# Performance work log

Measured on AMD Instinct MI355X. Metric: run time of the kernel, lower is better.

## Reference

```python
import jax, jax.numpy as jnp
import numpy as np

EPS = 1e-10      # normalizer eps from the torch module
IN_EPS = 1e-5    # torch InstanceNorm2d default eps
STRIDE = 2
PAD = 1


def _dw_conv_transpose(x, W):
    """Depthwise ConvTranspose2d applied for every output channel at once.

    x: [B, Cin, H, W]
    W: [Cin, Cout, kh, kw]  (W[:, i] is sub_convs[i].weight of shape [Cin, 1, kh, kw])
    returns: [B, Cin, Cout, H', W'] where channel (c, i) = convT of x[:, c] with W[c, i].
    """
    Cin, Cout, kh, kw = W.shape
    # Transposed conv == dilated conv with spatially flipped kernel,
    # lhs_dilation = stride, padding = k - 1 - pad (output_padding = 0).
    rhs = jnp.flip(W, axis=(-2, -1)).reshape(Cin * Cout, 1, kh, kw)
    pad_h = (kh - 1 - PAD, kh - 1 - PAD)
    pad_w = (kw - 1 - PAD, kw - 1 - PAD)
    out = jax.lax.conv_general_dilated(
        x, rhs,
        window_strides=(1, 1),
        padding=(pad_h, pad_w),
        lhs_dilation=(STRIDE, STRIDE),
        dimension_numbers=('NCHW', 'OIHW', 'NCHW'),
        feature_group_count=Cin,
    )  # [B, Cin*Cout, H', W'], group-major: group c -> channels c*Cout:(c+1)*Cout
    B = x.shape[0]
    return out.reshape(B, Cin, Cout, out.shape[2], out.shape[3])


def setup_inputs() -> dict:
    key = jax.random.key(0)
    k1, k2, k3 = jax.random.split(key, 3)
    B, Cin, Cout, H, Wd, K = 2, 64, 64, 48, 48, 4
    x = jax.random.normal(k1, (B, Cin, H, Wd), dtype=jnp.float32)
    # Positive-leaning weights keep the normalizer (convT of ones) away from zero.
    W = 0.05 + 0.1 * jax.random.uniform(k2, (Cin, Cout, K, K), dtype=jnp.float32)
    bias = 0.02 * jax.random.normal(k3, (Cout,), dtype=jnp.float32)
    return {"x": x, "W": W, "bias": bias}


def reference(x, W, bias):
    # numerator: depthwise convT of the input for every (in_ch, out_ch) pair
    num = _dw_conv_transpose(x, W)                       # [B, Cin, Cout, H', W']
    # normalizer: same convT applied to ones (batch-independent -> batch of 1)
    den = _dw_conv_transpose(jnp.ones_like(x[:1]), W) + EPS  # [1, Cin, Cout, H', W']
    out = jnp.sum(num / den, axis=1) + bias[None, :, None, None]  # [B, Cout, H', W']
    # InstanceNorm2d (no affine, biased variance) over spatial dims per (b, c)
    mean = jnp.mean(out, axis=(2, 3), keepdims=True)
    var = jnp.var(out, axis=(2, 3), keepdims=True)
    return (out - mean) / jnp.sqrt(var + IN_EPS)
```

## Files before the change

### kernel.cpp

```cpp
#include <hip/hip_runtime.h>

#define BB    2
#define CIN   64
#define NI    64
#define HIN   48
#define WIN   48
#define HO    96
#define WO    96
#define EPSN  1e-10f
#define IN_EPS 1e-5f
#define IMG   (HO*WO)
#define NIMG  (BB*NI)

#define TW    52
#define TROWS 50
#define TILE  (TROWS*TW)

__device__ float g_F[NI * CIN * 16];
__device__ float g_R[NI * CIN * 16];

__global__ __launch_bounds__(256) void prep_kernel(const float* __restrict__ Wt) {
    const int e = blockIdx.x * 256 + threadIdx.x;
    const int i = e >> 6, c = e & 63;
    float w[16];
    const float* wp = Wt + ((size_t)c * NI + i) * 16;
#pragma unroll
    for (int j = 0; j < 16; ++j) w[j] = wp[j];
    float* F = g_F + (size_t)e * 16;
    float* R = g_R + (size_t)e * 16;
#pragma unroll
    for (int j = 0; j < 16; ++j) {
        const int py = (j >> 3) & 1, px = (j >> 2) & 1, a = (j >> 1) & 1, bb = j & 1;
        const int kh = py ? (a ? 2 : 0) : (a ? 3 : 1);
        const int kw = px ? (bb ? 2 : 0) : (bb ? 3 : 1);
        const int r0 = py ? 0 : 1, r1 = py ? 2 : 3;
        const int q0 = px ? 0 : 1, q1 = px ? 2 : 3;
        const float den = w[r0 * 4 + q0] + w[r0 * 4 + q1]
                        + w[r1 * 4 + q0] + w[r1 * 4 + q1];
        F[j] = w[kh * 4 + kw] / (den + EPSN);
        const int cy = j >> 2, cx = j & 3;
        const int THn[4] = {1, 2, 2, 1};
        const int THv[4][2] = {{1, 1}, {0, 2}, {1, 3}, {2, 2}};
        float den2 = 0.f;
        for (int aa = 0; aa < THn[cy]; ++aa)
            for (int bb2 = 0; bb2 < THn[cx]; ++bb2)
                den2 += w[THv[cy][aa] * 4 + THv[cx][bb2]];
        R[j] = 1.f / (den2 + EPSN);
    }
}

template <int CS>
__global__ __launch_bounds__(192, 2) void conv_kernel(
        const float* __restrict__ x, const float* __restrict__ Wt,
        const float* __restrict__ bias, float* __restrict__ part) {
    constexpr int NC = CIN / CS;
    const int bi = blockIdx.x, s = blockIdx.y;
    const int b = bi >> 6, i = bi & 63, c0 = s * NC;
    const int tid = threadIdx.x;
    const int ty = tid / 12, tx = tid - 12 * ty;

    __shared__ __align__(16) float sX[2][TILE];
    __shared__ float sW[NC * 16];
    __shared__ float sR[NC * 16];
    __shared__ float sFix[384];

    {
        const float4 z = make_float4(0.f, 0.f, 0.f, 0.f);
        for (int e = tid; e < 2 * TROWS; e += 192) {
            const int q = e / TROWS, row = e - q * TROWS;
            float* rp = &sX[q][row * TW];
            if (row == 0 || row == TROWS - 1) {
#pragma unroll
                for (int k = 0; k < TW; k += 4) *(float4*)(rp + k) = z;
            } else {
                *(float4*)(rp + 48) = z;
            }
        }
    }
    for (int e = tid; e < NC * 16; e += 192) {
        const int c = e >> 4, j = e & 15;
        sW[e] = Wt[((size_t)(c0 + c) * NI + i) * 16 + j];
        sR[e] = g_R[((size_t)(i * CIN) + c0 + c) * 16 + j];
    }

    int ldsOff[3];
#pragma unroll
    for (int k = 0; k < 3; ++k) {
        const int e = tid + 192 * k;
        const int row = e / 12, c4 = e - 12 * row;
        ldsOff[k] = (row + 1) * TW + 4 * c4;
    }
    const float4* xg = (const float4*)x + (size_t)(b * CIN + c0) * 576;

    const int rowBase = 3 * ty;
    const int cMain = 4 * tx;
    const int cE0 = (tx == 0) ? 48 : 4 * tx - 1;
    const int cE5 = (tx == 11) ? 48 : 4 * tx + 4;

    int qA0[2], qA1[2], qB0[2], qB1[2], wI[2][4], clsI[2];
#pragma unroll
    for (int k = 0; k < 2; ++k) {
        const int p = tid + 192 * k;
        if (k == 1 && p >= 380) break;
        int y, xo;
        if (p < 96)       { y = 0;            xo = p; }
        else if (p < 192) { y = 95;           xo = p - 96; }
        else if (p < 286) { y = p - 192 + 1;  xo = 0; }
        else              { y = p - 286 + 1;  xo = 95; }
        const int hA = (y + 1) >> 1, hB = hA - 1;
        const int khA = (y & 1) ? 0 : 1, khB = khA + 2;
        const int wA = (xo + 1) >> 1, wB = wA - 1;
        const int kwA = (xo & 1) ? 0 : 1, kwB = kwA + 2;
        const int colA = wA;
        const int colB = (wB < 0) ? 48 : wB;
        const int rA = (hA + 1) * TW, rB = (hB + 1) * TW;
        qA0[k] = rA + colA; qA1[k] = rA + colB;
        qB0[k] = rB + colA; qB1[k] = rB + colB;
        wI[k][0] = khA * 4 + kwA; wI[k][1] = khA * 4 + kwB;
        wI[k][2] = khB * 4 + kwA; wI[k][3] = khB * 4 + kwB;
        const int cy = (y == 0) ? 0 : (y == 95) ? 3 : ((y & 1) ? 1 : 2);
        const int cx = (xo == 0) ? 0 : (xo == 95) ? 3 : ((xo & 1) ? 1 : 2);
        clsI[k] = cy * 4 + cx;
    }

    {
        const float4 a0 = xg[tid], a1 = xg[tid + 192], a2 = xg[tid + 384];
        float* d = &sX[0][0];
        *(float4*)(d + ldsOff[0]) = a0;
        *(float4*)(d + ldsOff[1]) = a1;
        *(float4*)(d + ldsOff[2]) = a2;
    }
    __syncthreads();

    float acc[6][8];
#pragma unroll
    for (int r = 0; r < 6; ++r)
#pragma unroll
        for (int j = 0; j < 8; ++j) acc[r][j] = 0.f;
    float fixAcc0 = 0.f, fixAcc1 = 0.f;

    const float* Fg = g_F + ((size_t)(i * CIN) + c0) * 16;

#pragma unroll 2
    for (int c = 0; c < NC; ++c) {
        float4 a0, a1, a2;
        if (c + 1 < NC) {
            const float4* xn = xg + (size_t)(c + 1) * 576;
            a0 = xn[tid]; a1 = xn[tid + 192]; a2 = xn[tid + 384];
        }

        float g[16];
        {
            const float* fp = Fg + c * 16;
#pragma unroll
            for (int k = 0; k < 16; ++k) g[k] = fp[k];
        }

        const float* __restrict__ xs = &sX[c & 1][0];

        float xv[5][6];
#pragma unroll
        for (int pr = 0; pr < 5; ++pr) {
            const int ro = (rowBase + pr) * TW;
            xv[pr][0] = xs[ro + cE0];
            const float4 m = *(const float4*)(xs + ro + cMain);
            xv[pr][1] = m.x; xv[pr][2] = m.y; xv[pr][3] = m.z; xv[pr][4] = m.w;
            xv[pr][5] = xs[ro + cE5];
        }

#pragma unroll
        for (int r = 0; r < 6; ++r) {
            const int prA = ((r + 1) >> 1) + 1, prB = prA - 1;
            const int py = r & 1;
#pragma unroll
            for (int j = 0; j < 8; ++j) {
                const int pcA = ((j + 1) >> 1) + 1, pcB = pcA - 1;
                const int px = j & 1;
                const float* gg = &g[py * 8 + px * 4];
                acc[r][j] += xv[prA][pcA] * gg[0] + xv[prA][pcB] * gg[1]
                           + xv[prB][pcA] * gg[2] + xv[prB][pcB] * gg[3];
            }
        }

        {
            const float* wc = &sW[c * 16];
            const float num0 = xs[qA0[0]] * wc[wI[0][0]] + xs[qA1[0]] * wc[wI[0][1]]
                             + xs[qB0[0]] * wc[wI[0][2]] + xs[qB1[0]] * wc[wI[0][3]];
            fixAcc0 += num0 * sR[c * 16 + clsI[0]];
            if (tid < 188) {
                const float num1 = xs[qA0[1]] * wc[wI[1][0]] + xs[qA1[1]] * wc[wI[1][1]]
                                 + xs[qB0[1]] * wc[wI[1][2]] + xs[qB1[1]] * wc[wI[1][3]];
                fixAcc1 += num1 * sR[c * 16 + clsI[1]];
            }
        }

        if (c + 1 < NC) {
            float* d = &sX[(c + 1) & 1][0];
            *(float4*)(d + ldsOff[0]) = a0;
            *(float4*)(d + ldsOff[1]) = a1;
            *(float4*)(d + ldsOff[2]) = a2;
        }
        __syncthreads();
    }

    sFix[tid] = fixAcc0;
    if (tid < 188) sFix[192 + tid] = fixAcc1;
    __syncthreads();

#pragma unroll
    for (int r = 0; r < 6; ++r)
#pragma unroll
        for (int j = 0; j < 8; ++j) {
            const int y = 6 * ty + r, xo = 8 * tx + j;
            if (y == 0)        acc[r][j] = sFix[xo];
            else if (y == 95)  acc[r][j] = sFix[96 + xo];
            else if (xo == 0)  acc[r][j] = sFix[192 + y - 1];
            else if (xo == 95) acc[r][j] = sFix[286 + y - 1];
        }

    const float bvq = bias[i] * (1.f / CS);
    float* pp = part + ((size_t)s * NIMG + bi) * IMG + (6 * ty) * WO + 8 * tx;
#pragma unroll
    for (int r = 0; r < 6; ++r) {
#pragma unroll
        for (int h = 0; h < 2; ++h) {
            float4 v;
            v.x = acc[r][4 * h]     + bvq;
            v.y = acc[r][4 * h + 1] + bvq;
            v.z = acc[r][4 * h + 2] + bvq;
            v.w = acc[r][4 * h + 3] + bvq;
            *(float4*)(pp + r * WO + 4 * h) = v;
        }
    }
}

template <int CS>
__global__ __launch_bounds__(768) void epilogue_kernel(
        const float* __restrict__ part, float* __restrict__ out) {
    const int bi = blockIdx.x;
    const int tid = threadIdx.x;
    const float4* pb = (const float4*)part + (size_t)bi * (IMG / 4);
    const size_t stride4 = (size_t)NIMG * (IMG / 4);

    float4 v[3];
    float s1 = 0.f, s2 = 0.f;
#pragma unroll
    for (int k = 0; k < 3; ++k) {
        const int idx = k * 768 + tid;
        float4 t = pb[idx];
#pragma unroll
        for (int s = 1; s < CS; ++s) {
            const float4 q = pb[s * stride4 + idx];
            t.x += q.x; t.y += q.y; t.z += q.z; t.w += q.w;
        }
        v[k] = t;
        s1 += t.x + t.y + t.z + t.w;
        s2 += t.x * t.x + t.y * t.y + t.z * t.z + t.w * t.w;
    }

    __shared__ float red[24];
    __shared__ float stat[2];
#pragma unroll
    for (int off = 32; off > 0; off >>= 1) {
        s1 += __shfl_down(s1, off, 64);
        s2 += __shfl_down(s2, off, 64);
    }
    const int w = tid >> 6;
    if ((tid & 63) == 0) { red[w] = s1; red[12 + w] = s2; }
    __syncthreads();
    if (tid == 0) {
        float t1 = 0.f, t2 = 0.f;
#pragma unroll
        for (int k = 0; k < 12; ++k) { t1 += red[k]; t2 += red[12 + k]; }
        const float mean = t1 * (1.f / 9216.f);
        const float m2 = t2 * (1.f / 9216.f);
        stat[0] = mean;
        stat[1] = rsqrtf(m2 - mean * mean + IN_EPS);
    }
    __syncthreads();
    const float mean = stat[0], inv = stat[1];

    float4* ob = (float4*)out + (size_t)bi * (IMG / 4);
#pragma unroll
    for (int k = 0; k < 3; ++k) {
        const int idx = k * 768 + tid;
        float4 t = v[k];
        t.x = (t.x - mean) * inv; t.y = (t.y - mean) * inv;
        t.z = (t.z - mean) * inv; t.w = (t.w - mean) * inv;
        ob[idx] = t;
    }
}

extern "C" void kernel_launch(void* const* d_in, const int* in_sizes, int n_in,
                              void* d_out, int out_size, void* d_ws, size_t ws_size,
                              hipStream_t stream) {
    const float* x    = (const float*)d_in[0];
    const float* Wt   = (const float*)d_in[1];
    const float* bias = (const float*)d_in[2];
    float* out = (float*)d_out;
    float* ws  = (float*)d_ws;

    prep_kernel<<<16, 256, 0, stream>>>(Wt);

    const size_t need4 = (size_t)4 * NIMG * IMG * 4;
    if (ws_size >= need4) {
        conv_kernel<4><<<dim3(NIMG, 4), 192, 0, stream>>>(x, Wt, bias, ws);
        epilogue_kernel<4><<<NIMG, 768, 0, stream>>>(ws, out);
    } else {
        conv_kernel<1><<<dim3(NIMG, 1), 192, 0, stream>>>(x, Wt, bias, out);
        epilogue_kernel<1><<<NIMG, 768, 0, stream>>>(out, out);
    }
}
```

Baseline: 94.73 us.

## Fuse weight prep into conv kernel and store split-K partials as fp16

Removes the separate prep kernel by computing the normalized weights F and reciprocal normalizers R per block into shared memory. Split-K partial sums are now written as half2 into a static device buffer instead of fp32 workspace, which halves the partial-sum traffic between the conv and epilogue kernels. Bias is added once in the epilogue. The fp16 partials lose precision before instance normalization, and the fallback path for a small workspace is dropped.

Measured after the change: 87.04 us. 8.1% less time.

```diff
diff --git a/kernel.cpp b/kernel.cpp
--- a/kernel.cpp
+++ b/kernel.cpp
@@ -1,4 +1,5 @@
 #include <hip/hip_runtime.h>
+#include <hip/hip_fp16.h>
 
 #define BB    2
 #define CIN   64
@@ -11,76 +12,63 @@
 #define IN_EPS 1e-5f
 #define IMG   (HO*WO)
 #define NIMG  (BB*NI)
+#define CS    4
+#define NC    (CIN/CS)
 
 #define TW    52
 #define TROWS 50
 #define TILE  (TROWS*TW)
 
-__device__ float g_F[NI * CIN * 16];
-__device__ float g_R[NI * CIN * 16];
-
-__global__ __launch_bounds__(256) void prep_kernel(const float* __restrict__ Wt) {
-    const int e = blockIdx.x * 256 + threadIdx.x;
-    const int i = e >> 6, c = e & 63;
-    float w[16];
-    const float* wp = Wt + ((size_t)c * NI + i) * 16;
-#pragma unroll
-    for (int j = 0; j < 16; ++j) w[j] = wp[j];
-    float* F = g_F + (size_t)e * 16;
-    float* R = g_R + (size_t)e * 16;
-#pragma unroll
-    for (int j = 0; j < 16; ++j) {
+__device__ __align__(16) __half2 g_part[CS * NIMG * (IMG / 2)];
+
+__global__ __launch_bounds__(192, 2) void conv_kernel(
+        const float* __restrict__ x, const float* __restrict__ Wt,
+        float* __restrict__ unused) {
+    const int bi = blockIdx.x, s = blockIdx.y;
+    const int b = bi >> 6, i = bi & 63, c0 = s * NC;
+    const int tid = threadIdx.x;
+    const int ty = tid / 12, tx = tid - 12 * ty;
+
+    __shared__ __align__(16) float sX[2][TILE];
+    __shared__ __align__(16) float sF[NC * 16];
+    __shared__ float sW[NC * 16];
+    __shared__ float sR[NC * 16];
+    __shared__ float sFix[384];
+
+    {
+        const float4 z = make_float4(0.f, 0.f, 0.f, 0.f);
+        for (int e = tid; e < 2 * TROWS; e += 192) {
+            const int q = e / TROWS, row = e - q * TROWS;
+            float* rp = &sX[q][row * TW];
+            if (row == 0 || row == TROWS - 1) {
+#pragma unroll
+                for (int k = 0; k < TW; k += 4) *(float4*)(rp + k) = z;
+            } else {
+                *(float4*)(rp + 48) = z;
+            }
+        }
+    }
+
+    for (int e = tid; e < NC * 16; e += 192) {
+        const int c = e >> 4, j = e & 15;
+        const float* wp = Wt + ((size_t)(c0 + c) * NI + i) * 16;
+        sW[e] = wp[j];
         const int py = (j >> 3) & 1, px = (j >> 2) & 1, a = (j >> 1) & 1, bb = j & 1;
         const int kh = py ? (a ? 2 : 0) : (a ? 3 : 1);
         const int kw = px ? (bb ? 2 : 0) : (bb ? 3 : 1);
         const int r0 = py ? 0 : 1, r1 = py ? 2 : 3;
         const int q0 = px ? 0 : 1, q1 = px ? 2 : 3;
-        const float den = w[r0 * 4 + q0] + w[r0 * 4 + q1]
-                        + w[r1 * 4 + q0] + w[r1 * 4 + q1];
-        F[j] = w[kh * 4 + kw] / (den + EPSN);
+        const float den = wp[r0 * 4 + q0] + wp[r0 * 4 + q1]
+                        + wp[r1 * 4 + q0] + wp[r1 * 4 + q1];
+        sF[e] = wp[kh * 4 + kw] / (den + EPSN);
         const int cy = j >> 2, cx = j & 3;
         const int THn[4] = {1, 2, 2, 1};
         const int THv[4][2] = {{1, 1}, {0, 2}, {1, 3}, {2, 2}};
         float den2 = 0.f;
         for (int aa = 0; aa < THn[cy]; ++aa)
             for (int bb2 = 0; bb2 < THn[cx]; ++bb2)
-                den2 += w[THv[cy][aa] * 4 + THv[cx][bb2]];
-        R[j] = 1.f / (den2 + EPSN);
-    }
-}
-
-template <int CS>
-__global__ __launch_bounds__(192, 2) void conv_kernel(
-        const float* __restrict__ x, const float* __restrict__ Wt,
-        const float* __restrict__ bias, float* __restrict__ part) {
-    constexpr int NC = CIN / CS;
-    const int bi = blockIdx.x, s = blockIdx.y;
-    const int b = bi >> 6, i = bi & 63, c0 = s * NC;
-    const int tid = threadIdx.x;
-    const int ty = tid / 12, tx = tid - 12 * ty;
-
-    __shared__ __align__(16) float sX[2][TILE];
-    __shared__ float sW[NC * 16];
-    __shared__ float sR[NC * 16];
-    __shared__ float sFix[384];
-
-    {
-        const float4 z = make_float4(0.f, 0.f, 0.f, 0.f);
-        for (int e = tid; e < 2 * TROWS; e += 192) {
-            const int q = e / TROWS, row = e - q * TROWS;
-            float* rp = &sX[q][row * TW];
-            if (row == 0 || row == TROWS - 1) {
-#pragma unroll
-                for (int k = 0; k < TW; k += 4) *(float4*)(rp + k) = z;
-            } else {
-                *(float4*)(rp + 48) = z;
-            }
-        }
-    }
-    for (int e = tid; e < NC * 16; e += 192) {
-        const int c = e >> 4, j = e & 15;
-        sW[e] = Wt[((size_t)(c0 + c) * NI + i) * 16 + j];
-        sR[e] = g_R[((size_t)(i * CIN) + c0 + c) * 16 + j];
+                den2 += wp[THv[cy][aa] * 4 + THv[cx][bb2]];
+        sR[e] = 1.f / (den2 + EPSN);
     }
 
     int ldsOff[3];
@@ -123,6 +111,8 @@
         clsI[k] = cy * 4 + cx;
     }
 
+    __syncthreads();
+
     {
         const float4 a0 = xg[tid], a1 = xg[tid + 192], a2 = xg[tid + 384];
         float* d = &sX[0][0];
@@ -139,8 +129,6 @@
         for (int j = 0; j < 8; ++j) acc[r][j] = 0.f;
     float fixAcc0 = 0.f, fixAcc1 = 0.f;
 
-    const float* Fg = g_F + ((size_t)(i * CIN) + c0) * 16;
-
 #pragma unroll 2
     for (int c = 0; c < NC; ++c) {
         float4 a0, a1, a2;
@@ -151,9 +139,13 @@
 
         float g[16];
         {
-            const float* fp = Fg + c * 16;
-#pragma unroll
-            for (int k = 0; k < 16; ++k) g[k] = fp[k];
+            const float4* gf = (const float4*)&sF[c * 16];
+#pragma unroll
+            for (int q = 0; q < 4; ++q) {
+                const float4 t = gf[q];
+                g[4 * q] = t.x; g[4 * q + 1] = t.y;
+                g[4 * q + 2] = t.z; g[4 * q + 3] = t.w;
+            }
         }
 
         const float* __restrict__ xs = &sX[c & 1][0];
@@ -218,41 +210,45 @@
             else if (xo == 95) acc[r][j] = sFix[286 + y - 1];
         }
 
-    const float bvq = bias[i] * (1.f / CS);
-    float* pp = part + ((size_t)s * NIMG + bi) * IMG + (6 * ty) * WO + 8 * tx;
-#pragma unroll
-    for (int r = 0; r < 6; ++r) {
-#pragma unroll
-        for (int h = 0; h < 2; ++h) {
-            float4 v;
-            v.x = acc[r][4 * h]     + bvq;
-            v.y = acc[r][4 * h + 1] + bvq;
-            v.z = acc[r][4 * h + 2] + bvq;
-            v.w = acc[r][4 * h + 3] + bvq;
-            *(float4*)(pp + r * WO + 4 * h) = v;
+    {
+        __half2* pp = g_part + ((size_t)s * NIMG + bi) * (IMG / 2)
+                    + (6 * ty) * (WO / 2) + 4 * tx;
+#pragma unroll
+        for (int r = 0; r < 6; ++r) {
+            __half2 h[4];
+#pragma unroll
+            for (int q = 0; q < 4; ++q)
+                h[q] = __floats2half2_rn(acc[r][2 * q], acc[r][2 * q + 1]);
+            *(float4*)(pp + r * (WO / 2)) = *(float4*)h;
         }
     }
 }
 
-template <int CS>
 __global__ __launch_bounds__(768) void epilogue_kernel(
-        const float* __restrict__ part, float* __restrict__ out) {
+        const float* __restrict__ bias, float* __restrict__ out) {
     const int bi = blockIdx.x;
     const int tid = threadIdx.x;
-    const float4* pb = (const float4*)part + (size_t)bi * (IMG / 4);
-    const size_t stride4 = (size_t)NIMG * (IMG / 4);
+    const float bv = bias[bi & 63];
+    const __half2* pb = g_part + (size_t)bi * (IMG / 2);
+    const size_t stride2 = (size_t)NIMG * (IMG / 2);
 
     float4 v[3];
     float s1 = 0.f, s2 = 0.f;
 #pragma unroll
     for (int k = 0; k < 3; ++k) {
-        const int idx = k * 768 + tid;
-        float4 t = pb[idx];
-#pragma unroll
-        for (int s = 1; s < CS; ++s) {
-            const float4 q = pb[s * stride4 + idx];
-            t.x += q.x; t.y += q.y; t.z += q.z; t.w += q.w;
-        }
+        const int idx2 = (k * 768 + tid) * 2;
+        float ax = 0.f, ay = 0.f, az = 0.f, aw = 0.f;
+#pragma unroll
+        for (int sp = 0; sp < CS; ++sp) {
+            const float2 raw = *(const float2*)(pb + sp * stride2 + idx2);
+            const __half2 h0 = ((const __half2*)&raw)[0];
+            const __half2 h1 = ((const __half2*)&raw)[1];
+            const float2 f0 = __half22float2(h0);
+            const float2 f1 = __half22float2(h1);
+            ax += f0.x; ay += f0.y; az += f1.x; aw += f1.y;
+        }
+        float4 t;
+        t.x = ax + bv; t.y = ay + bv; t.z = az + bv; t.w = aw + bv;
         v[k] = t;
         s1 += t.x + t.y + t.z + t.w;
         s2 += t.x * t.x + t.y * t.y + t.z * t.z + t.w * t.w;
@@ -298,16 +294,8 @@
     const float* Wt   = (const float*)d_in[1];
     const float* bias = (const float*)d_in[2];
     float* out = (float*)d_out;
-    float* ws  = (float*)d_ws;
-
-    prep_kernel<<<16, 256, 0, stream>>>(Wt);
-
-    const size_t need4 = (size_t)4 * NIMG * IMG * 4;
-    if (ws_size >= need4) {
-        conv_kernel<4><<<dim3(NIMG, 4), 192, 0, stream>>>(x, Wt, bias, ws);
-        epilogue_kernel<4><<<NIMG, 768, 0, stream>>>(ws, out);
-    } else {
-        conv_kernel<1><<<dim3(NIMG, 1), 192, 0, stream>>>(x, Wt, bias, out);
-        epilogue_kernel<1><<<NIMG, 768, 0, stream>>>(out, out);
-    }
+    (void)d_ws; (void)ws_size;
+
+    conv_kernel<<<dim3(NIMG, CS), 192, 0, stream>>>(x, Wt, nullptr);
+    epilogue_kernel<<<NIMG, 768, 0, stream>>>(bias, out);
 }
```
